# Optimization experiments

Measured on AMD Instinct MI355X. Metric: run time of the kernel, lower is better.

## Reference

```python
import jax, jax.numpy as jnp
import numpy as np

N = 50000
E = 800000
F_IN = 256
HID = 64
HEADS = 4
CLASSES = 32
NEG_SLOPE = 0.2


def setup_inputs() -> dict:
    key = jax.random.key(0)
    ks = jax.random.split(key, 10)
    x = jax.random.normal(ks[0], (N, F_IN), dtype=jnp.float32)
    edge_index = jax.random.randint(ks[1], (2, E), 0, N, dtype=jnp.int64)
    s1 = 1.0 / np.sqrt(F_IN)
    s2 = 1.0 / np.sqrt(HID * HEADS)
    W1 = jax.random.normal(ks[2], (F_IN, HEADS * HID), dtype=jnp.float32) * s1
    a_src1 = jax.random.normal(ks[3], (HEADS, HID), dtype=jnp.float32) * s1
    a_dst1 = jax.random.normal(ks[4], (HEADS, HID), dtype=jnp.float32) * s1
    b1 = jnp.zeros((HEADS * HID,), dtype=jnp.float32)
    W2 = jax.random.normal(ks[5], (HEADS * HID, CLASSES), dtype=jnp.float32) * s2
    a_src2 = jax.random.normal(ks[6], (1, CLASSES), dtype=jnp.float32) * s2
    a_dst2 = jax.random.normal(ks[7], (1, CLASSES), dtype=jnp.float32) * s2
    b2 = jnp.zeros((CLASSES,), dtype=jnp.float32)
    return {"x": x, "edge_index": edge_index, "W1": W1, "a_src1": a_src1,
            "a_dst1": a_dst1, "b1": b1, "W2": W2, "a_src2": a_src2,
            "a_dst2": a_dst2, "b2": b2}


def gat_conv(x, src, dst, W, a_src, a_dst, bias, num_nodes):
    # PyG GATConv: h = x W, per-head attention logits, segment softmax over dst,
    # scatter-weighted aggregation. src/dst already include self-loops.
    H, C = a_src.shape
    h = (x @ W).reshape(num_nodes, H, C)               # [N, H, C]
    al_s = jnp.sum(h * a_src[None], axis=-1)            # [N, H]
    al_d = jnp.sum(h * a_dst[None], axis=-1)            # [N, H]
    e = jax.nn.leaky_relu(al_s[src] + al_d[dst], NEG_SLOPE)  # [Et, H]
    m = jax.ops.segment_max(e, dst, num_segments=num_nodes)  # [N, H]
    ex = jnp.exp(e - m[dst])
    denom = jax.ops.segment_sum(ex, dst, num_segments=num_nodes)
    alpha = ex / denom[dst]                              # [Et, H]
    out = jax.ops.segment_sum(alpha[:, :, None] * h[src], dst,
                              num_segments=num_nodes)    # [N, H, C]
    return out.reshape(num_nodes, H * C) + bias


def reference(x, edge_index, W1, a_src1, a_dst1, b1, W2, a_src2, a_dst2, b2):
    num_nodes = x.shape[0]
    loop = jnp.arange(num_nodes, dtype=edge_index.dtype)
    src = jnp.concatenate([edge_index[0], loop])  # add_self_loops=True (PyG default)
    dst = jnp.concatenate([edge_index[1], loop])
    # dropout is identity in eval mode
    h = jax.nn.elu(gat_conv(x, src, dst, W1, a_src1, a_dst1, b1, num_nodes))
    out = gat_conv(h, src, dst, W2, a_src2, a_dst2, b2, num_nodes)
    return jax.nn.log_softmax(out, axis=1)
```

## Files before the change

### kernel.cpp

```cpp
#include <hip/hip_runtime.h>
#include <math.h>

#define N_NODES 50000
#define N_EDGES 800000
#define NEG_SLOPE 0.2f
#define PADU N_NODES
#define LOG2E 1.44269504088896f

#define BSHIFT 8
#define NBUK ((N_NODES + 255) >> BSHIFT)
#define BCAP 4608
#define ACHUNK 4096
#define PADBUK 5632
#define ET_PAD_ALLOC (NBUK * PADBUK)

typedef __attribute__((ext_vector_type(8))) short s16x8;
typedef __attribute__((ext_vector_type(4))) float f32x4;
typedef __attribute__((ext_vector_type(2))) float f32x2;

__device__ __forceinline__ unsigned short f2bf(float f) {
    union { float f; unsigned u; } v; v.f = f;
    unsigned r = v.u + 0x7FFF + ((v.u >> 16) & 1);
    return (unsigned short)(r >> 16);
}
__device__ __forceinline__ float asf(unsigned u) {
    union { unsigned u; float f; } v; v.u = u;
    return v.f;
}
__device__ __forceinline__ uint4 pack_bf16_trunc(float4 f0, float4 f1) {
    const unsigned* a = (const unsigned*)&f0;
    const unsigned* b = (const unsigned*)&f1;
    uint4 r;
    r.x = (a[0] >> 16) | (a[1] & 0xffff0000u);
    r.y = (a[2] >> 16) | (a[3] & 0xffff0000u);
    r.z = (b[0] >> 16) | (b[1] & 0xffff0000u);
    r.w = (b[2] >> 16) | (b[3] & 0xffff0000u);
    return r;
}
__device__ __forceinline__ unsigned char f2fp8(float f) {
    return (unsigned char)(__builtin_amdgcn_cvt_pk_fp8_f32(f, f, 0, false) & 0xff);
}


__global__ __launch_bounds__(256) void k_cvtw(const float* __restrict__ W1, const float* __restrict__ W2,
                                              unsigned short* __restrict__ WT, unsigned short* __restrict__ W2T,
                                              int* __restrict__ bcur, float* __restrict__ als1,
                                              unsigned char* __restrict__ H8) {
    int b = blockIdx.x, k = threadIdx.x;
    if (b < 256) {
        WT[b * 256 + k] = f2bf(W1[k * 256 + b]);
    } else if (b < 288) {
        int c = b - 256;
        W2T[c * 256 + k] = f2bf(W2[k * 32 + c]);
    } else {
        if (k < NBUK) bcur[k] = 0;
        if (k >= 196 && k < 200) als1[N_NODES * 4 + (k - 196)] = -1e30f;
        if (k >= 200 && k < 264) {
            int w = k - 200;
            int plane = w >> 4, wi = w & 15;
            ((unsigned*)H8)[((size_t)plane * (N_NODES + 1) + N_NODES) * 16 + wi] = 0;
        }
    }
}


__global__ __launch_bounds__(256) void k_bin(const int* __restrict__ ei, int* __restrict__ bcur,
                                             unsigned* __restrict__ stage) {
    __shared__ unsigned sdata[ACHUNK];
    __shared__ unsigned short sv[ACHUNK];
    __shared__ int scnt[NBUK];
    __shared__ int soff[NBUK + 1];
    __shared__ int sgbase[NBUK];
    __shared__ int wssc[4];
    int tid = threadIdx.x;
    int e0 = blockIdx.x * ACHUNK;
    int nE = N_EDGES - e0;
    if (nE > ACHUNK) nE = ACHUNK;
    for (int i = tid; i < NBUK; i += 256) scnt[i] = 0;
    __syncthreads();
    for (int i = tid; i < nE; i += 256) {
        int v = ei[N_EDGES + e0 + i];
        sv[i] = (unsigned short)v;
        atomicAdd(&scnt[v >> BSHIFT], 1);
    }
    __syncthreads();
    {
        int lane = tid & 63, w = tid >> 6;
        int val = (tid < NBUK) ? scnt[tid] : 0;
        int incl = val;
        for (int o = 1; o < 64; o <<= 1) {
            int t = __shfl_up(incl, o);
            if (lane >= o) incl += t;
        }
        if (lane == 63) wssc[w] = incl;
        __syncthreads();
        int wb = 0;
        for (int i = 0; i < w; ++i) wb += wssc[i];
        if (tid < NBUK) soff[tid] = wb + incl - val;
        if (tid == 255) soff[NBUK] = wb + incl;
    }
    __syncthreads();
    if (tid < NBUK) {
        int c = scnt[tid];
        sgbase[tid] = c ? atomicAdd(&bcur[tid], c) : 0;
        scnt[tid] = soff[tid];
    }
    __syncthreads();
    for (int i = tid; i < nE; i += 256) {
        int u = ei[e0 + i];
        unsigned v = sv[i];
        int b = (int)(v >> BSHIFT);
        int pos = atomicAdd(&scnt[b], 1);
        sdata[pos] = (unsigned)u | ((v & 255u) << 16) | ((unsigned)b << 24);
    }
    __syncthreads();
    for (int i = tid; i < nE; i += 256) {
        unsigned pk = sdata[i];
        int buk = (int)(pk >> 24);
        int rel = sgbase[buk] + (i - soff[buk]);
        if (rel < BCAP) stage[(size_t)buk * BCAP + rel] = pk;
    }
}


__global__ __launch_bounds__(256) void k_build(const unsigned* __restrict__ stage,
                                               const int* __restrict__ bcur,
                                               int* __restrict__ offp, int* __restrict__ ecnt,
                                               unsigned short* __restrict__ esrc) {
    __shared__ int hist[256];
    __shared__ int lexcl[257];
    __shared__ int ws[4];
    __shared__ int outbuf[PADBUK];
    int b = blockIdx.x, tid = threadIdx.x;
    int n = bcur[b];
    if (n > BCAP) n = BCAP;
    int base = b << BSHIFT;
    int nv = N_NODES - base;
    if (nv > 256) nv = 256;
    hist[tid] = 0;
    __syncthreads();
    const unsigned* sg = stage + (size_t)b * BCAP;
    for (int i = tid; i < n; i += 256) atomicAdd(&hist[(sg[i] >> 16) & 0xFF], 1);
    __syncthreads();
    int lane = tid & 63, w = tid >> 6;
    int c = (tid < nv) ? hist[tid] + 1 : 0;
    int r = (tid < nv) ? ((c + 3) & ~3) : 0;
    int incl = r;
    for (int o = 1; o < 64; o <<= 1) {
        int t = __shfl_up(incl, o);
        if (lane >= o) incl += t;
    }
    if (lane == 63) ws[w] = incl;
    __syncthreads();
    int wb = 0;
    for (int i = 0; i < w; ++i) wb += ws[i];
    int excl = wb + incl - r;
    lexcl[tid] = excl;
    if (tid == 255) lexcl[256] = excl + r;
    int gb = b * PADBUK;
    if (tid < nv) {
        offp[base + tid] = gb + excl;
        ecnt[base + tid] = c;
    }
    __syncthreads();
    int total = lexcl[256];
    if (tid < nv) {
        outbuf[excl] = base + tid;
        for (int j = excl + c; j < excl + r; ++j) outbuf[j] = PADU;
        hist[tid] = 1;
    }
    __syncthreads();
    for (int i = tid; i < n; i += 256) {
        unsigned pk = sg[i];
        int vloc = (int)((pk >> 16) & 0xFF);
        int pos = lexcl[vloc] + atomicAdd(&hist[vloc], 1);
        outbuf[pos] = (int)(pk & 0xffffu);
    }
    __syncthreads();
    for (int i = tid; i < total; i += 256) esrc[gb + i] = (unsigned short)outbuf[i];
}


__global__ __launch_bounds__(256) void k_gemm1m(const float* __restrict__ X, const unsigned short* __restrict__ WT,
                                                const float* __restrict__ a_src, const float* __restrict__ a_dst,
                                                unsigned char* __restrict__ H8,
                                                float* __restrict__ als, float* __restrict__ ald) {
    __shared__ unsigned short As[64][40];
    __shared__ unsigned short Bs[256][40];
    int tid = threadIdx.x;
    int row0 = blockIdx.x * 64;
    int wv = tid >> 6, lane = tid & 63;
    int wm = wv & 1, wn = wv >> 1;
    int lr = lane & 15, quad = lane >> 4;
    f32x4 acc[2][8];
#pragma unroll
    for (int mt = 0; mt < 2; ++mt)
#pragma unroll
        for (int nt = 0; nt < 8; ++nt) acc[mt][nt] = (f32x4){0.f, 0.f, 0.f, 0.f};

    int ar = tid >> 2, aseg = tid & 3;
    for (int k0 = 0; k0 < 256; k0 += 32) {
        {
            int grow = row0 + ar;
            float4 f0 = make_float4(0.f, 0.f, 0.f, 0.f), f1 = f0;
            if (grow < N_NODES) {
                const float* src = X + (size_t)grow * 256 + k0 + aseg * 8;
                f0 = *(const float4*)src;
                f1 = *(const float4*)(src + 4);
            }
            *(uint4*)&As[ar][aseg * 8] = pack_bf16_trunc(f0, f1);
        }
#pragma unroll
        for (int pass = 0; pass < 4; ++pass) {
            int q = tid + pass * 256;
            int n = q >> 2, seg = q & 3;
            uint4 v = *(const uint4*)(WT + (n << 8) + k0 + seg * 8);
            *(uint4*)&Bs[n][seg * 8] = v;
        }
        __syncthreads();
        s16x8 a[2], b[8];
#pragma unroll
        for (int mt = 0; mt < 2; ++mt) a[mt] = *(const s16x8*)&As[wm * 32 + mt * 16 + lr][quad * 8];
#pragma unroll
        for (int nt = 0; nt < 8; ++nt) b[nt] = *(const s16x8*)&Bs[wn * 128 + nt * 16 + lr][quad * 8];
#pragma unroll
        for (int mt = 0; mt < 2; ++mt)
#pragma unroll
            for (int nt = 0; nt < 8; ++nt)
                acc[mt][nt] = __builtin_amdgcn_mfma_f32_16x16x32_bf16(a[mt], b[nt], acc[mt][nt], 0, 0, 0);
        __syncthreads();
    }
#pragma unroll
    for (int mt = 0; mt < 2; ++mt) {
#pragma unroll
        for (int r = 0; r < 4; ++r) {
            int row = row0 + wm * 32 + mt * 16 + quad * 4 + r;
            if (row < N_NODES) {
#pragma unroll
                for (int nt = 0; nt < 8; ++nt) {
                    int col = wn * 128 + nt * 16 + lr;
                    int plane = col >> 6;
                    H8[((size_t)plane * (N_NODES + 1) + row) * 64 + (col & 63)] = f2fp8(acc[mt][nt][r]);
                }
            }
        }
    }
    float av[8], dv[8];
#pragma unroll
    for (int nt = 0; nt < 8; ++nt) {
        int col = wn * 128 + nt * 16 + lr;
        av[nt] = a_src[col] * LOG2E;
        dv[nt] = a_dst[col] * LOG2E;
    }
    float ps[2][8], pd[2][8];
#pragma unroll
    for (int hl = 0; hl < 2; ++hl)
#pragma unroll
        for (int i = 0; i < 8; ++i) { ps[hl][i] = 0.f; pd[hl][i] = 0.f; }
#pragma unroll
    for (int mt = 0; mt < 2; ++mt)
#pragma unroll
        for (int nt = 0; nt < 8; ++nt) {
            int hl = nt >> 2;
#pragma unroll
            for (int r = 0; r < 4; ++r) {
                float v = acc[mt][nt][r];
                ps[hl][mt * 4 + r] = fmaf(v, av[nt], ps[hl][mt * 4 + r]);
                pd[hl][mt * 4 + r] = fmaf(v, dv[nt], pd[hl][mt * 4 + r]);
            }
        }
#pragma unroll
    for (int hl = 0; hl < 2; ++hl)
#pragma unroll
        for (int i = 0; i < 8; ++i) {
            float s = ps[hl][i], d = pd[hl][i];
#pragma unroll
            for (int m = 8; m >= 1; m >>= 1) { s += __shfl_xor(s, m); d += __shfl_xor(d, m); }
            if (lr == 0) {
                int row = row0 + wm * 32 + (i >> 2) * 16 + quad * 4 + (i & 3);
                if (row < N_NODES) {
                    als[row * 4 + wn * 2 + hl] = s;
                    ald[row * 4 + wn * 2 + hl] = d;
                }
            }
        }
}


__global__ __launch_bounds__(256) void k_agg1(const unsigned* __restrict__ H8u,
                                              const float* __restrict__ als, const float* __restrict__ ald_,
                                              const int* __restrict__ offp, const int* __restrict__ ecnt,
                                              const unsigned short* __restrict__ esrc,
                                              const float* __restrict__ b1, unsigned* __restrict__ H2p) {
    int tid = threadIdx.x;
    int head = blockIdx.x & 3;
    int node = (blockIdx.x >> 2) * 16 + (tid >> 4);
    int lane16 = tid & 15;
    const unsigned* Hp = H8u + (size_t)head * (N_NODES + 1) * 16;
    float ald = ald_[node * 4 + head];
    int pstart = offp[node];
    int rend = pstart + ((ecnt[node] + 3) & ~3);
    float l = 0.f;
    f32x2 axy = (f32x2){0.f, 0.f}, azw = (f32x2){0.f, 0.f};

    auto quad = [&](unsigned ua, unsigned ub) {
        int u0 = (int)(ua & 0xffffu), u1 = (int)(ua >> 16);
        int u2 = (int)(ub & 0xffffu), u3 = (int)(ub >> 16);
        unsigned v0 = Hp[(unsigned)u0 * 16 + lane16];
        unsigned v1 = Hp[(unsigned)u1 * 16 + lane16];
        unsigned v2 = Hp[(unsigned)u2 * 16 + lane16];
        unsigned v3 = Hp[(unsigned)u3 * 16 + lane16];
        f32x2 e01 = (f32x2){als[u0 * 4 + head], als[u1 * 4 + head]} + (f32x2){ald, ald};
        f32x2 e23 = (f32x2){als[u2 * 4 + head], als[u3 * 4 + head]} + (f32x2){ald, ald};
        f32x2 t01 = e01 * NEG_SLOPE, t23 = e23 * NEG_SLOPE;
        float e0 = fmaxf(e01.x, t01.x), e1 = fmaxf(e01.y, t01.y);
        float e2 = fmaxf(e23.x, t23.x), e3 = fmaxf(e23.y, t23.y);
        float pw0 = __builtin_amdgcn_exp2f(e0);
        float pw1 = __builtin_amdgcn_exp2f(e1);
        float pw2 = __builtin_amdgcn_exp2f(e2);
        float pw3 = __builtin_amdgcn_exp2f(e3);
        l += (pw0 + pw1) + (pw2 + pw3);
        f32x2 a0 = __builtin_amdgcn_cvt_pk_f32_fp8(v0, false), b0 = __builtin_amdgcn_cvt_pk_f32_fp8(v0, true);
        f32x2 a1 = __builtin_amdgcn_cvt_pk_f32_fp8(v1, false), b1v = __builtin_amdgcn_cvt_pk_f32_fp8(v1, true);
        f32x2 a2 = __builtin_amdgcn_cvt_pk_f32_fp8(v2, false), b2v = __builtin_amdgcn_cvt_pk_f32_fp8(v2, true);
        f32x2 a3 = __builtin_amdgcn_cvt_pk_f32_fp8(v3, false), b3v = __builtin_amdgcn_cvt_pk_f32_fp8(v3, true);
        axy += (f32x2){pw0, pw0} * a0;
        azw += (f32x2){pw0, pw0} * b0;
        axy += (f32x2){pw1, pw1} * a1;
        azw += (f32x2){pw1, pw1} * b1v;
        axy += (f32x2){pw2, pw2} * a2;
        azw += (f32x2){pw2, pw2} * b2v;
        axy += (f32x2){pw3, pw3} * a3;
        azw += (f32x2){pw3, pw3} * b3v;
    };

    int p = pstart;
    for (; p + 7 < rend; p += 8) {
        uint2 ua = *(const uint2*)(esrc + p);
        uint2 ub = *(const uint2*)(esrc + p + 4);
        quad(ua.x, ua.y);
        quad(ub.x, ub.y);
    }
    if (p < rend) {
        uint2 ua = *(const uint2*)(esrc + p);
        quad(ua.x, ua.y);
    }

    float inv = 1.f / l;
    int ell = head * 16 + lane16;
    float4 bb = *(const float4*)(b1 + ell * 4);
    float o0 = axy.x * inv + bb.x, o1 = axy.y * inv + bb.y, o2 = azw.x * inv + bb.z, o3 = azw.y * inv + bb.w;
    o0 = o0 > 0.f ? o0 : expm1f(o0);
    o1 = o1 > 0.f ? o1 : expm1f(o1);
    o2 = o2 > 0.f ? o2 : expm1f(o2);
    o3 = o3 > 0.f ? o3 : expm1f(o3);
    unsigned pk = __builtin_amdgcn_cvt_pk_fp8_f32(o0, o1, 0, false);
    pk = __builtin_amdgcn_cvt_pk_fp8_f32(o2, o3, pk, true);
    H2p[(unsigned)node * 64 + ell] = pk;
}


__global__ __launch_bounds__(256) void k_gemm2m(const unsigned* __restrict__ H2p,
                                                const unsigned short* __restrict__ W2T,
                                                const float* __restrict__ as2, const float* __restrict__ ad2,
                                                unsigned short* __restrict__ Gb, float* __restrict__ als2,
                                                float* __restrict__ ald2) {
    int tid = threadIdx.x;
    int wv = tid >> 6, lane = tid & 63, lr = lane & 15, quad = lane >> 4;
    int row0 = blockIdx.x * 64 + wv * 16;
    int rowA = row0 + lr;
    unsigned rA = (rowA < N_NODES) ? (unsigned)rowA : (unsigned)(N_NODES - 1);
    f32x4 acc[2];
    acc[0] = (f32x4){0.f, 0.f, 0.f, 0.f};
    acc[1] = (f32x4){0.f, 0.f, 0.f, 0.f};
#pragma unroll
    for (int k0 = 0; k0 < 256; k0 += 32) {
        uint2 d = *(const uint2*)(H2p + rA * 64 + (k0 >> 2) + quad * 2);
        f32x2 f0 = __builtin_amdgcn_cvt_pk_f32_fp8(d.x, false);
        f32x2 f1 = __builtin_amdgcn_cvt_pk_f32_fp8(d.x, true);
        f32x2 f2 = __builtin_amdgcn_cvt_pk_f32_fp8(d.y, false);
        f32x2 f3 = __builtin_amdgcn_cvt_pk_f32_fp8(d.y, true);
        union { uint4 u; s16x8 s; } cv;
        cv.u = pack_bf16_trunc(make_float4(f0.x, f0.y, f1.x, f1.y), make_float4(f2.x, f2.y, f3.x, f3.y));
        s16x8 afrag = cv.s;
        s16x8 b0 = *(const s16x8*)(W2T + lr * 256 + k0 + quad * 8);
        s16x8 b1f = *(const s16x8*)(W2T + (16 + lr) * 256 + k0 + quad * 8);
        acc[0] = __builtin_amdgcn_mfma_f32_16x16x32_bf16(afrag, b0, acc[0], 0, 0, 0);
        acc[1] = __builtin_amdgcn_mfma_f32_16x16x32_bf16(afrag, b1f, acc[1], 0, 0, 0);
    }
    float a2s = as2[lr] * LOG2E, a2s2 = as2[16 + lr] * LOG2E;
    float a2d = ad2[lr] * LOG2E, a2d2 = ad2[16 + lr] * LOG2E;
#pragma unroll
    for (int r = 0; r < 4; ++r) {
        int row = row0 + quad * 4 + r;
        float g0 = acc[0][r], g1 = acc[1][r];
        float s = g0 * a2s + g1 * a2s2;
        float dd = g0 * a2d + g1 * a2d2;
#pragma unroll
        for (int m = 8; m >= 1; m >>= 1) { s += __shfl_xor(s, m); dd += __shfl_xor(dd, m); }
        if (row < N_NODES) {
            Gb[(size_t)row * 32 + lr] = f2bf(g0);
            Gb[(size_t)row * 32 + 16 + lr] = f2bf(g1);
            if (lr == 0) { als2[row] = s; ald2[row] = dd; }
        }
    }
}


__global__ __launch_bounds__(256) void k_agg2(const unsigned short* __restrict__ Gb,
                                              const float* __restrict__ als2,
                                              const float* __restrict__ ald2_, const int* __restrict__ offp,
                                              const int* __restrict__ ecnt,
                                              const unsigned short* __restrict__ esrc, const float* __restrict__ b2,
                                              float* __restrict__ out) {
    int gid = blockIdx.x * 256 + threadIdx.x;
    int node = gid >> 4;
    int colp = gid & 15;
    if (node >= N_NODES) return;
    float ald = ald2_[node];
    int pstart = offp[node];
    int pend = pstart + ecnt[node];
    float l = 0.f;
    f32x2 accv = (f32x2){0.f, 0.f};

    auto edge1 = [&](int u0) {
        unsigned gpk = *(const unsigned*)(Gb + (size_t)(unsigned)u0 * 32 + 2 * colp);
        f32x2 g01 = (f32x2){asf(gpk << 16), asf(gpk & 0xffff0000u)};
        float e0 = als2[u0] + ald;
        e0 = fmaxf(e0, NEG_SLOPE * e0);
        float pw0 = __builtin_amdgcn_exp2f(e0);
        l += pw0;
        accv += (f32x2){pw0, pw0} * g01;
    };
    auto quad = [&](unsigned ua, unsigned ub) {
        int u0 = (int)(ua & 0xffffu), u1 = (int)(ua >> 16);
        int u2 = (int)(ub & 0xffffu), u3 = (int)(ub >> 16);
        unsigned g0p = *(const unsigned*)(Gb + (size_t)(unsigned)u0 * 32 + 2 * colp);
        unsigned g1p = *(const unsigned*)(Gb + (size_t)(unsigned)u1 * 32 + 2 * colp);
        unsigned g2p = *(const unsigned*)(Gb + (size_t)(unsigned)u2 * 32 + 2 * colp);
        unsigned g3p = *(const unsigned*)(Gb + (size_t)(unsigned)u3 * 32 + 2 * colp);
        f32x2 e01 = (f32x2){als2[u0], als2[u1]} + (f32x2){ald, ald};
        f32x2 e23 = (f32x2){als2[u2], als2[u3]} + (f32x2){ald, ald};
        f32x2 t01 = e01 * NEG_SLOPE, t23 = e23 * NEG_SLOPE;
        float e0 = fmaxf(e01.x, t01.x), e1 = fmaxf(e01.y, t01.y);
        float e2 = fmaxf(e23.x, t23.x), e3 = fmaxf(e23.y, t23.y);
        float pw0 = __builtin_amdgcn_exp2f(e0), pw1 = __builtin_amdgcn_exp2f(e1);
        float pw2 = __builtin_amdgcn_exp2f(e2), pw3 = __builtin_amdgcn_exp2f(e3);
        l += (pw0 + pw1) + (pw2 + pw3);
        f32x2 g0 = (f32x2){asf(g0p << 16), asf(g0p & 0xffff0000u)};
        f32x2 g1 = (f32x2){asf(g1p << 16), asf(g1p & 0xffff0000u)};
        f32x2 g2 = (f32x2){asf(g2p << 16), asf(g2p & 0xffff0000u)};
        f32x2 g3 = (f32x2){asf(g3p << 16), asf(g3p & 0xffff0000u)};
        accv += (f32x2){pw0, pw0} * g0;
        accv += (f32x2){pw1, pw1} * g1;
        accv += (f32x2){pw2, pw2} * g2;
        accv += (f32x2){pw3, pw3} * g3;
    };

    int p = pstart;
    for (; p + 7 < pend; p += 8) {
        uint2 ua = *(const uint2*)(esrc + p);
        uint2 ub = *(const uint2*)(esrc + p + 4);
        quad(ua.x, ua.y);
        quad(ub.x, ub.y);
    }
    for (; p + 3 < pend; p += 4) {
        uint2 ua = *(const uint2*)(esrc + p);
        quad(ua.x, ua.y);
    }
    for (; p < pend; ++p) edge1(esrc[p]);

    float inv = 1.f / l;
    float2 bb = *(const float2*)(b2 + 2 * colp);
    float o0 = accv.x * inv + bb.x;
    float o1 = accv.y * inv + bb.y;
    float mm = fmaxf(o0, o1);
#pragma unroll
    for (int msk = 8; msk >= 1; msk >>= 1) mm = fmaxf(mm, __shfl_xor(mm, msk));
    float s = __expf(o0 - mm) + __expf(o1 - mm);
#pragma unroll
    for (int msk = 8; msk >= 1; msk >>= 1) s += __shfl_xor(s, msk);
    float ls = logf(s);
    float2 res = make_float2(o0 - mm - ls, o1 - mm - ls);
    *(float2*)(out + (size_t)node * 32 + 2 * colp) = res;
}


extern "C" void kernel_launch(void* const* d_in, const int* in_sizes, int n_in,
                              void* d_out, int out_size, void* d_ws, size_t ws_size,
                              hipStream_t stream) {
    const float* x   = (const float*)d_in[0];
    const int*   ei  = (const int*)d_in[1];
    const float* W1  = (const float*)d_in[2];
    const float* as1 = (const float*)d_in[3];
    const float* ad1 = (const float*)d_in[4];
    const float* b1  = (const float*)d_in[5];
    const float* W2  = (const float*)d_in[6];
    const float* as2 = (const float*)d_in[7];
    const float* ad2 = (const float*)d_in[8];
    const float* b2  = (const float*)d_in[9];
    float* out = (float*)d_out;

    char* p = (char*)d_ws;
    auto alloc = [&](size_t bytes) {
        char* r = p;
        p += (bytes + 255) & ~(size_t)255;
        return r;
    };
    unsigned char*  h8  = (unsigned char*)alloc((size_t)(N_NODES + 1) * 256);
    unsigned char*  h2pr= (unsigned char*)alloc((size_t)N_NODES * 64 * 4);
    unsigned short* wt  = (unsigned short*)alloc((size_t)256 * 256 * 2);
    unsigned short* w2t = (unsigned short*)alloc((size_t)32 * 256 * 2);
    float* als1 = (float*)alloc(((size_t)N_NODES * 4 + 4) * 4);
    float* ald1 = (float*)alloc((size_t)N_NODES * 4 * 4);
    float* als2 = (float*)alloc((size_t)N_NODES * 4);
    float* ald2 = (float*)alloc((size_t)N_NODES * 4);
    int* bcur    = (int*)alloc(256 * 4);
    int* offp = (int*)alloc((size_t)N_NODES * 4);
    int* ecnt = (int*)alloc((size_t)N_NODES * 4);
    unsigned short* esrc = (unsigned short*)alloc((size_t)ET_PAD_ALLOC * 2);

    unsigned* stage = (unsigned*)h2pr;
    unsigned* h2p = (unsigned*)h2pr;
    unsigned short* g = (unsigned short*)h8;

    k_cvtw<<<289, 256, 0, stream>>>(W1, W2, wt, w2t, bcur, als1, h8);
    k_bin<<<(N_EDGES + ACHUNK - 1) / ACHUNK, 256, 0, stream>>>(ei, bcur, stage);
    k_build<<<NBUK, 256, 0, stream>>>(stage, bcur, offp, ecnt, esrc);

    k_gemm1m<<<(N_NODES + 63) / 64, 256, 0, stream>>>(x, wt, as1, ad1, h8, als1, ald1);
    k_agg1<<<(N_NODES / 16) * 4, 256, 0, stream>>>((const unsigned*)h8, als1, ald1, offp, ecnt, esrc, b1, h2p);
    k_gemm2m<<<(N_NODES + 63) / 64, 256, 0, stream>>>(h2p, w2t, as2, ad2, g, als2, ald2);
    k_agg2<<<(N_NODES * 16 + 255) / 256, 256, 0, stream>>>(g, als2, ald2, offp, ecnt, esrc, b2, out);
}
```

Before: 227.9 us.

## Store layer-1 features node-major and aggregate all heads per node in one pass

The fp8 hidden features change from head-planar storage to one contiguous 256-byte row per node. The first aggregation kernel now assigns 32 lanes per node covering all four heads, with each lane loading 8 bytes. Previously there was one block per head, and every head re-read the node's edge list, offsets and attention inputs. The new scheme walks the edge list once per node and gathers full contiguous neighbor rows, at the cost of more accumulator registers and more per-lane work.

```diff
diff --git a/kernel.cpp b/kernel.cpp
--- a/kernel.cpp
+++ b/kernel.cpp
@@ -55,11 +55,7 @@
     } else {
         if (k < NBUK) bcur[k] = 0;
         if (k >= 196 && k < 200) als1[N_NODES * 4 + (k - 196)] = -1e30f;
-        if (k >= 200 && k < 264) {
-            int w = k - 200;
-            int plane = w >> 4, wi = w & 15;
-            ((unsigned*)H8)[((size_t)plane * (N_NODES + 1) + N_NODES) * 16 + wi] = 0;
-        }
+        if (k >= 200 && k < 264) ((unsigned*)H8)[(size_t)N_NODES * 64 + (k - 200)] = 0;
     }
 }
 
@@ -239,8 +235,7 @@
 #pragma unroll
                 for (int nt = 0; nt < 8; ++nt) {
                     int col = wn * 128 + nt * 16 + lr;
-                    int plane = col >> 6;
-                    H8[((size_t)plane * (N_NODES + 1) + row) * 64 + (col & 63)] = f2fp8(acc[mt][nt][r]);
+                    H8[(size_t)row * 256 + col] = f2fp8(acc[mt][nt][r]);
                 }
             }
         }
@@ -287,29 +282,31 @@
 }
 
 
-__global__ __launch_bounds__(256) void k_agg1(const unsigned* __restrict__ H8u,
+__global__ __launch_bounds__(256) void k_agg1(const uint2* __restrict__ H8u2,
                                               const float* __restrict__ als, const float* __restrict__ ald_,
                                               const int* __restrict__ offp, const int* __restrict__ ecnt,
                                               const unsigned short* __restrict__ esrc,
-                                              const float* __restrict__ b1, unsigned* __restrict__ H2p) {
+                                              const float* __restrict__ b1, uint2* __restrict__ H2p2) {
     int tid = threadIdx.x;
-    int head = blockIdx.x & 3;
-    int node = (blockIdx.x >> 2) * 16 + (tid >> 4);
-    int lane16 = tid & 15;
-    const unsigned* Hp = H8u + (size_t)head * (N_NODES + 1) * 16;
+    int wid = (blockIdx.x * 256 + tid) >> 6;
+    int half = (tid >> 5) & 1;
+    int node = wid * 2 + half;
+    int lane = tid & 31;
+    int head = lane >> 3;
     float ald = ald_[node * 4 + head];
     int pstart = offp[node];
     int rend = pstart + ((ecnt[node] + 3) & ~3);
     float l = 0.f;
-    f32x2 axy = (f32x2){0.f, 0.f}, azw = (f32x2){0.f, 0.f};
+    f32x2 acc0 = (f32x2){0.f, 0.f}, acc1 = (f32x2){0.f, 0.f};
+    f32x2 acc2 = (f32x2){0.f, 0.f}, acc3 = (f32x2){0.f, 0.f};
 
     auto quad = [&](unsigned ua, unsigned ub) {
         int u0 = (int)(ua & 0xffffu), u1 = (int)(ua >> 16);
         int u2 = (int)(ub & 0xffffu), u3 = (int)(ub >> 16);
-        unsigned v0 = Hp[(unsigned)u0 * 16 + lane16];
-        unsigned v1 = Hp[(unsigned)u1 * 16 + lane16];
-        unsigned v2 = Hp[(unsigned)u2 * 16 + lane16];
-        unsigned v3 = Hp[(unsigned)u3 * 16 + lane16];
+        uint2 v0 = H8u2[(unsigned)u0 * 32 + lane];
+        uint2 v1 = H8u2[(unsigned)u1 * 32 + lane];
+        uint2 v2 = H8u2[(unsigned)u2 * 32 + lane];
+        uint2 v3 = H8u2[(unsigned)u3 * 32 + lane];
         f32x2 e01 = (f32x2){als[u0 * 4 + head], als[u1 * 4 + head]} + (f32x2){ald, ald};
         f32x2 e23 = (f32x2){als[u2 * 4 + head], als[u3 * 4 + head]} + (f32x2){ald, ald};
         f32x2 t01 = e01 * NEG_SLOPE, t23 = e23 * NEG_SLOPE;
@@ -320,18 +317,24 @@
         float pw2 = __builtin_amdgcn_exp2f(e2);
         float pw3 = __builtin_amdgcn_exp2f(e3);
         l += (pw0 + pw1) + (pw2 + pw3);
-        f32x2 a0 = __builtin_amdgcn_cvt_pk_f32_fp8(v0, false), b0 = __builtin_amdgcn_cvt_pk_f32_fp8(v0, true);
-        f32x2 a1 = __builtin_amdgcn_cvt_pk_f32_fp8(v1, false), b1v = __builtin_amdgcn_cvt_pk_f32_fp8(v1, true);
-        f32x2 a2 = __builtin_amdgcn_cvt_pk_f32_fp8(v2, false), b2v = __builtin_amdgcn_cvt_pk_f32_fp8(v2, true);
-        f32x2 a3 = __builtin_amdgcn_cvt_pk_f32_fp8(v3, false), b3v = __builtin_amdgcn_cvt_pk_f32_fp8(v3, true);
-        axy += (f32x2){pw0, pw0} * a0;
-        azw += (f32x2){pw0, pw0} * b0;
-        axy += (f32x2){pw1, pw1} * a1;
-        azw += (f32x2){pw1, pw1} * b1v;
-        axy += (f32x2){pw2, pw2} * a2;
-        azw += (f32x2){pw2, pw2} * b2v;
-        axy += (f32x2){pw3, pw3} * a3;
-        azw += (f32x2){pw3, pw3} * b3v;
+        f32x2 w0 = (f32x2){pw0, pw0}, w1 = (f32x2){pw1, pw1};
+        f32x2 w2 = (f32x2){pw2, pw2}, w3 = (f32x2){pw3, pw3};
+        acc0 += w0 * __builtin_amdgcn_cvt_pk_f32_fp8(v0.x, false);
+        acc1 += w0 * __builtin_amdgcn_cvt_pk_f32_fp8(v0.x, true);
+        acc2 += w0 * __builtin_amdgcn_cvt_pk_f32_fp8(v0.y, false);
+        acc3 += w0 * __builtin_amdgcn_cvt_pk_f32_fp8(v0.y, true);
+        acc0 += w1 * __builtin_amdgcn_cvt_pk_f32_fp8(v1.x, false);
+        acc1 += w1 * __builtin_amdgcn_cvt_pk_f32_fp8(v1.x, true);
+        acc2 += w1 * __builtin_amdgcn_cvt_pk_f32_fp8(v1.y, false);
+        acc3 += w1 * __builtin_amdgcn_cvt_pk_f32_fp8(v1.y, true);
+        acc0 += w2 * __builtin_amdgcn_cvt_pk_f32_fp8(v2.x, false);
+        acc1 += w2 * __builtin_amdgcn_cvt_pk_f32_fp8(v2.x, true);
+        acc2 += w2 * __builtin_amdgcn_cvt_pk_f32_fp8(v2.y, false);
+        acc3 += w2 * __builtin_amdgcn_cvt_pk_f32_fp8(v2.y, true);
+        acc0 += w3 * __builtin_amdgcn_cvt_pk_f32_fp8(v3.x, false);
+        acc1 += w3 * __builtin_amdgcn_cvt_pk_f32_fp8(v3.x, true);
+        acc2 += w3 * __builtin_amdgcn_cvt_pk_f32_fp8(v3.y, false);
+        acc3 += w3 * __builtin_amdgcn_cvt_pk_f32_fp8(v3.y, true);
     };
 
     int p = pstart;
@@ -347,16 +350,26 @@
     }
 
     float inv = 1.f / l;
-    int ell = head * 16 + lane16;
-    float4 bb = *(const float4*)(b1 + ell * 4);
-    float o0 = axy.x * inv + bb.x, o1 = axy.y * inv + bb.y, o2 = azw.x * inv + bb.z, o3 = azw.y * inv + bb.w;
+    int c = lane * 8;
+    float4 bb0 = *(const float4*)(b1 + c);
+    float4 bb1 = *(const float4*)(b1 + c + 4);
+    float o0 = acc0.x * inv + bb0.x, o1 = acc0.y * inv + bb0.y;
+    float o2 = acc1.x * inv + bb0.z, o3 = acc1.y * inv + bb0.w;
+    float o4 = acc2.x * inv + bb1.x, o5 = acc2.y * inv + bb1.y;
+    float o6 = acc3.x * inv + bb1.z, o7 = acc3.y * inv + bb1.w;
     o0 = o0 > 0.f ? o0 : expm1f(o0);
     o1 = o1 > 0.f ? o1 : expm1f(o1);
     o2 = o2 > 0.f ? o2 : expm1f(o2);
     o3 = o3 > 0.f ? o3 : expm1f(o3);
-    unsigned pk = __builtin_amdgcn_cvt_pk_fp8_f32(o0, o1, 0, false);
-    pk = __builtin_amdgcn_cvt_pk_fp8_f32(o2, o3, pk, true);
-    H2p[(unsigned)node * 64 + ell] = pk;
+    o4 = o4 > 0.f ? o4 : expm1f(o4);
+    o5 = o5 > 0.f ? o5 : expm1f(o5);
+    o6 = o6 > 0.f ? o6 : expm1f(o6);
+    o7 = o7 > 0.f ? o7 : expm1f(o7);
+    unsigned pkx = __builtin_amdgcn_cvt_pk_fp8_f32(o0, o1, 0, false);
+    pkx = __builtin_amdgcn_cvt_pk_fp8_f32(o2, o3, pkx, true);
+    unsigned pky = __builtin_amdgcn_cvt_pk_fp8_f32(o4, o5, 0, false);
+    pky = __builtin_amdgcn_cvt_pk_fp8_f32(o6, o7, pky, true);
+    H2p2[(unsigned)node * 32 + lane] = make_uint2(pkx, pky);
 }
 
 
@@ -529,7 +542,8 @@
     k_build<<<NBUK, 256, 0, stream>>>(stage, bcur, offp, ecnt, esrc);
 
     k_gemm1m<<<(N_NODES + 63) / 64, 256, 0, stream>>>(x, wt, as1, ad1, h8, als1, ald1);
-    k_agg1<<<(N_NODES / 16) * 4, 256, 0, stream>>>((const unsigned*)h8, als1, ald1, offp, ecnt, esrc, b1, h2p);
+    k_agg1<<<(N_NODES / 2 + 3) / 4, 256, 0, stream>>>((const uint2*)h8, als1, ald1, offp, ecnt, esrc, b1,
+                                                      (uint2*)h2p);
     k_gemm2m<<<(N_NODES + 63) / 64, 256, 0, stream>>>(h2p, w2t, as2, ad2, g, als2, ald2);
     k_agg2<<<(N_NODES * 16 + 255) / 256, 256, 0, stream>>>(g, als2, ald2, offp, ecnt, esrc, b2, out);
 }
```

After: 216.3 us. -5.1%, faster.

## Use row-major fp8 H layout with 16-byte gathers in both aggregation kernels

Applied to the files above, without the earlier changes.

The first-layer projected features move from a per-head planar fp8 layout to a contiguous row-major layout of 256 bytes per node. k_agg1 now handles all four heads of a node with 16 lanes each loading a uint4, instead of one head per block with 4-byte loads, and it writes its output as uint4. k_agg2 uses 8 lanes per node with 8-byte loads instead of 16 lanes with 4-byte loads, halving its thread count. Wider gathers mean fewer memory transactions and fewer redundant edge-index and logit reads, at the cost of more registers per thread and less thread-level parallelism.

```diff
diff --git a/kernel.cpp b/kernel.cpp
--- a/kernel.cpp
+++ b/kernel.cpp
@@ -55,11 +55,7 @@
     } else {
         if (k < NBUK) bcur[k] = 0;
         if (k >= 196 && k < 200) als1[N_NODES * 4 + (k - 196)] = -1e30f;
-        if (k >= 200 && k < 264) {
-            int w = k - 200;
-            int plane = w >> 4, wi = w & 15;
-            ((unsigned*)H8)[((size_t)plane * (N_NODES + 1) + N_NODES) * 16 + wi] = 0;
-        }
+        if (k >= 200 && k < 264) ((unsigned*)H8)[(size_t)N_NODES * 64 + (k - 200)] = 0;
     }
 }
 
@@ -239,8 +235,7 @@
 #pragma unroll
                 for (int nt = 0; nt < 8; ++nt) {
                     int col = wn * 128 + nt * 16 + lr;
-                    int plane = col >> 6;
-                    H8[((size_t)plane * (N_NODES + 1) + row) * 64 + (col & 63)] = f2fp8(acc[mt][nt][r]);
+                    H8[(size_t)row * 256 + col] = f2fp8(acc[mt][nt][r]);
                 }
             }
         }
@@ -287,29 +282,43 @@
 }
 
 
-__global__ __launch_bounds__(256) void k_agg1(const unsigned* __restrict__ H8u,
+__global__ __launch_bounds__(256) void k_agg1(const uint4* __restrict__ H8u4,
                                               const float* __restrict__ als, const float* __restrict__ ald_,
                                               const int* __restrict__ offp, const int* __restrict__ ecnt,
                                               const unsigned short* __restrict__ esrc,
-                                              const float* __restrict__ b1, unsigned* __restrict__ H2p) {
+                                              const float* __restrict__ b1, uint4* __restrict__ H2p4) {
     int tid = threadIdx.x;
-    int head = blockIdx.x & 3;
-    int node = (blockIdx.x >> 2) * 16 + (tid >> 4);
-    int lane16 = tid & 15;
-    const unsigned* Hp = H8u + (size_t)head * (N_NODES + 1) * 16;
+    int wid = (blockIdx.x * 256 + tid) >> 6;
+    int grp = (tid >> 4) & 3;
+    int node = wid * 4 + grp;
+    int lane = tid & 15;
+    int head = lane >> 2;
     float ald = ald_[node * 4 + head];
     int pstart = offp[node];
     int rend = pstart + ((ecnt[node] + 3) & ~3);
     float l = 0.f;
-    f32x2 axy = (f32x2){0.f, 0.f}, azw = (f32x2){0.f, 0.f};
+    f32x2 acc[8];
+#pragma unroll
+    for (int i = 0; i < 8; ++i) acc[i] = (f32x2){0.f, 0.f};
+
+    auto accum = [&](uint4 v, f32x2 w) {
+        acc[0] += w * __builtin_amdgcn_cvt_pk_f32_fp8(v.x, false);
+        acc[1] += w * __builtin_amdgcn_cvt_pk_f32_fp8(v.x, true);
+        acc[2] += w * __builtin_amdgcn_cvt_pk_f32_fp8(v.y, false);
+        acc[3] += w * __builtin_amdgcn_cvt_pk_f32_fp8(v.y, true);
+        acc[4] += w * __builtin_amdgcn_cvt_pk_f32_fp8(v.z, false);
+        acc[5] += w * __builtin_amdgcn_cvt_pk_f32_fp8(v.z, true);
+        acc[6] += w * __builtin_amdgcn_cvt_pk_f32_fp8(v.w, false);
+        acc[7] += w * __builtin_amdgcn_cvt_pk_f32_fp8(v.w, true);
+    };
 
     auto quad = [&](unsigned ua, unsigned ub) {
         int u0 = (int)(ua & 0xffffu), u1 = (int)(ua >> 16);
         int u2 = (int)(ub & 0xffffu), u3 = (int)(ub >> 16);
-        unsigned v0 = Hp[(unsigned)u0 * 16 + lane16];
-        unsigned v1 = Hp[(unsigned)u1 * 16 + lane16];
-        unsigned v2 = Hp[(unsigned)u2 * 16 + lane16];
-        unsigned v3 = Hp[(unsigned)u3 * 16 + lane16];
+        uint4 v0 = H8u4[(unsigned)u0 * 16 + lane];
+        uint4 v1 = H8u4[(unsigned)u1 * 16 + lane];
+        uint4 v2 = H8u4[(unsigned)u2 * 16 + lane];
+        uint4 v3 = H8u4[(unsigned)u3 * 16 + lane];
         f32x2 e01 = (f32x2){als[u0 * 4 + head], als[u1 * 4 + head]} + (f32x2){ald, ald};
         f32x2 e23 = (f32x2){als[u2 * 4 + head], als[u3 * 4 + head]} + (f32x2){ald, ald};
         f32x2 t01 = e01 * NEG_SLOPE, t23 = e23 * NEG_SLOPE;
@@ -320,18 +329,10 @@
         float pw2 = __builtin_amdgcn_exp2f(e2);
         float pw3 = __builtin_amdgcn_exp2f(e3);
         l += (pw0 + pw1) + (pw2 + pw3);
-        f32x2 a0 = __builtin_amdgcn_cvt_pk_f32_fp8(v0, false), b0 = __builtin_amdgcn_cvt_pk_f32_fp8(v0, true);
-        f32x2 a1 = __builtin_amdgcn_cvt_pk_f32_fp8(v1, false), b1v = __builtin_amdgcn_cvt_pk_f32_fp8(v1, true);
-        f32x2 a2 = __builtin_amdgcn_cvt_pk_f32_fp8(v2, false), b2v = __builtin_amdgcn_cvt_pk_f32_fp8(v2, true);
-        f32x2 a3 = __builtin_amdgcn_cvt_pk_f32_fp8(v3, false), b3v = __builtin_amdgcn_cvt_pk_f32_fp8(v3, true);
-        axy += (f32x2){pw0, pw0} * a0;
-        azw += (f32x2){pw0, pw0} * b0;
-        axy += (f32x2){pw1, pw1} * a1;
-        azw += (f32x2){pw1, pw1} * b1v;
-        axy += (f32x2){pw2, pw2} * a2;
-        azw += (f32x2){pw2, pw2} * b2v;
-        axy += (f32x2){pw3, pw3} * a3;
-        azw += (f32x2){pw3, pw3} * b3v;
+        accum(v0, (f32x2){pw0, pw0});
+        accum(v1, (f32x2){pw1, pw1});
+        accum(v2, (f32x2){pw2, pw2});
+        accum(v3, (f32x2){pw3, pw3});
     };
 
     int p = pstart;
@@ -347,16 +348,23 @@
     }
 
     float inv = 1.f / l;
-    int ell = head * 16 + lane16;
-    float4 bb = *(const float4*)(b1 + ell * 4);
-    float o0 = axy.x * inv + bb.x, o1 = axy.y * inv + bb.y, o2 = azw.x * inv + bb.z, o3 = azw.y * inv + bb.w;
-    o0 = o0 > 0.f ? o0 : expm1f(o0);
-    o1 = o1 > 0.f ? o1 : expm1f(o1);
-    o2 = o2 > 0.f ? o2 : expm1f(o2);
-    o3 = o3 > 0.f ? o3 : expm1f(o3);
-    unsigned pk = __builtin_amdgcn_cvt_pk_fp8_f32(o0, o1, 0, false);
-    pk = __builtin_amdgcn_cvt_pk_fp8_f32(o2, o3, pk, true);
-    H2p[(unsigned)node * 64 + ell] = pk;
+    int c = lane * 16;
+    unsigned words[4];
+#pragma unroll
+    for (int j = 0; j < 4; ++j) {
+        float4 bb = *(const float4*)(b1 + c + 4 * j);
+        float p0 = acc[2 * j].x * inv + bb.x;
+        float p1 = acc[2 * j].y * inv + bb.y;
+        float p2 = acc[2 * j + 1].x * inv + bb.z;
+        float p3 = acc[2 * j + 1].y * inv + bb.w;
+        p0 = p0 > 0.f ? p0 : expm1f(p0);
+        p1 = p1 > 0.f ? p1 : expm1f(p1);
+        p2 = p2 > 0.f ? p2 : expm1f(p2);
+        p3 = p3 > 0.f ? p3 : expm1f(p3);
+        unsigned w = __builtin_amdgcn_cvt_pk_fp8_f32(p0, p1, 0, false);
+        words[j] = __builtin_amdgcn_cvt_pk_fp8_f32(p2, p3, w, true);
+    }
+    H2p4[(unsigned)node * 16 + lane] = make_uint4(words[0], words[1], words[2], words[3]);
 }
 
 
@@ -414,31 +422,35 @@
                                               const unsigned short* __restrict__ esrc, const float* __restrict__ b2,
                                               float* __restrict__ out) {
     int gid = blockIdx.x * 256 + threadIdx.x;
-    int node = gid >> 4;
-    int colp = gid & 15;
+    int node = gid >> 3;
+    int colp = gid & 7;
     if (node >= N_NODES) return;
     float ald = ald2_[node];
     int pstart = offp[node];
     int pend = pstart + ecnt[node];
     float l = 0.f;
-    f32x2 accv = (f32x2){0.f, 0.f};
-
+    f32x2 accv0 = (f32x2){0.f, 0.f}, accv1 = (f32x2){0.f, 0.f};
+
+    auto gload = [&](int u) {
+        return *(const uint2*)(Gb + (size_t)(unsigned)u * 32 + 4 * colp);
+    };
+    auto gacc = [&](uint2 gp, float pw) {
+        f32x2 w = (f32x2){pw, pw};
+        accv0 += w * (f32x2){asf(gp.x << 16), asf(gp.x & 0xffff0000u)};
+        accv1 += w * (f32x2){asf(gp.y << 16), asf(gp.y & 0xffff0000u)};
+    };
     auto edge1 = [&](int u0) {
-        unsigned gpk = *(const unsigned*)(Gb + (size_t)(unsigned)u0 * 32 + 2 * colp);
-        f32x2 g01 = (f32x2){asf(gpk << 16), asf(gpk & 0xffff0000u)};
+        uint2 gp = gload(u0);
         float e0 = als2[u0] + ald;
         e0 = fmaxf(e0, NEG_SLOPE * e0);
         float pw0 = __builtin_amdgcn_exp2f(e0);
         l += pw0;
-        accv += (f32x2){pw0, pw0} * g01;
+        gacc(gp, pw0);
     };
     auto quad = [&](unsigned ua, unsigned ub) {
         int u0 = (int)(ua & 0xffffu), u1 = (int)(ua >> 16);
         int u2 = (int)(ub & 0xffffu), u3 = (int)(ub >> 16);
-        unsigned g0p = *(const unsigned*)(Gb + (size_t)(unsigned)u0 * 32 + 2 * colp);
-        unsigned g1p = *(const unsigned*)(Gb + (size_t)(unsigned)u1 * 32 + 2 * colp);
-        unsigned g2p = *(const unsigned*)(Gb + (size_t)(unsigned)u2 * 32 + 2 * colp);
-        unsigned g3p = *(const unsigned*)(Gb + (size_t)(unsigned)u3 * 32 + 2 * colp);
+        uint2 g0 = gload(u0), g1 = gload(u1), g2 = gload(u2), g3 = gload(u3);
         f32x2 e01 = (f32x2){als2[u0], als2[u1]} + (f32x2){ald, ald};
         f32x2 e23 = (f32x2){als2[u2], als2[u3]} + (f32x2){ald, ald};
         f32x2 t01 = e01 * NEG_SLOPE, t23 = e23 * NEG_SLOPE;
@@ -447,14 +459,10 @@
         float pw0 = __builtin_amdgcn_exp2f(e0), pw1 = __builtin_amdgcn_exp2f(e1);
         float pw2 = __builtin_amdgcn_exp2f(e2), pw3 = __builtin_amdgcn_exp2f(e3);
         l += (pw0 + pw1) + (pw2 + pw3);
-        f32x2 g0 = (f32x2){asf(g0p << 16), asf(g0p & 0xffff0000u)};
-        f32x2 g1 = (f32x2){asf(g1p << 16), asf(g1p & 0xffff0000u)};
-        f32x2 g2 = (f32x2){asf(g2p << 16), asf(g2p & 0xffff0000u)};
-        f32x2 g3 = (f32x2){asf(g3p << 16), asf(g3p & 0xffff0000u)};
-        accv += (f32x2){pw0, pw0} * g0;
-        accv += (f32x2){pw1, pw1} * g1;
-        accv += (f32x2){pw2, pw2} * g2;
-        accv += (f32x2){pw3, pw3} * g3;
+        gacc(g0, pw0);
+        gacc(g1, pw1);
+        gacc(g2, pw2);
+        gacc(g3, pw3);
     };
 
     int p = pstart;
@@ -471,18 +479,20 @@
     for (; p < pend; ++p) edge1(esrc[p]);
 
     float inv = 1.f / l;
-    float2 bb = *(const float2*)(b2 + 2 * colp);
-    float o0 = accv.x * inv + bb.x;
-    float o1 = accv.y * inv + bb.y;
-    float mm = fmaxf(o0, o1);
-#pragma unroll
-    for (int msk = 8; msk >= 1; msk >>= 1) mm = fmaxf(mm, __shfl_xor(mm, msk));
-    float s = __expf(o0 - mm) + __expf(o1 - mm);
-#pragma unroll
-    for (int msk = 8; msk >= 1; msk >>= 1) s += __shfl_xor(s, msk);
+    float4 bb = *(const float4*)(b2 + 4 * colp);
+    float o0 = accv0.x * inv + bb.x;
+    float o1 = accv0.y * inv + bb.y;
+    float o2 = accv1.x * inv + bb.z;
+    float o3 = accv1.y * inv + bb.w;
+    float mm = fmaxf(fmaxf(o0, o1), fmaxf(o2, o3));
+#pragma unroll
+    for (int msk = 4; msk >= 1; msk >>= 1) mm = fmaxf(mm, __shfl_xor(mm, msk));
+    float s = (__expf(o0 - mm) + __expf(o1 - mm)) + (__expf(o2 - mm) + __expf(o3 - mm));
+#pragma unroll
+    for (int msk = 4; msk >= 1; msk >>= 1) s += __shfl_xor(s, msk);
     float ls = logf(s);
-    float2 res = make_float2(o0 - mm - ls, o1 - mm - ls);
-    *(float2*)(out + (size_t)node * 32 + 2 * colp) = res;
+    float4 res = make_float4(o0 - mm - ls, o1 - mm - ls, o2 - mm - ls, o3 - mm - ls);
+    *(float4*)(out + (size_t)node * 32 + 4 * colp) = res;
 }
 
 
@@ -529,7 +539,8 @@
     k_build<<<NBUK, 256, 0, stream>>>(stage, bcur, offp, ecnt, esrc);
 
     k_gemm1m<<<(N_NODES + 63) / 64, 256, 0, stream>>>(x, wt, as1, ad1, h8, als1, ald1);
-    k_agg1<<<(N_NODES / 16) * 4, 256, 0, stream>>>((const unsigned*)h8, als1, ald1, offp, ecnt, esrc, b1, h2p);
+    k_agg1<<<(N_NODES * 16) / 256, 256, 0, stream>>>((const uint4*)h8, als1, ald1, offp, ecnt, esrc, b1,
+                                                     (uint4*)h2p);
     k_gemm2m<<<(N_NODES + 63) / 64, 256, 0, stream>>>(h2p, w2t, as2, ad2, g, als2, ald2);
-    k_agg2<<<(N_NODES * 16 + 255) / 256, 256, 0, stream>>>(g, als2, ald2, offp, ecnt, esrc, b2, out);
-}
+    k_agg2<<<(N_NODES * 8 + 255) / 256, 256, 0, stream>>>(g, als2, ald2, offp, ecnt, esrc, b2, out);
+}
```

After: 221.7 us. 1.03x faster.
